# Performance work log

Hardware: AMD Instinct MI355X
Metric: run time of the kernel (lower is better)

Reference implementation:

```python
import jax, jax.numpy as jnp
import numpy as np

N = 20000; F = 2000; H1 = 256; H2 = 64; E = 320000
BN_EPS = 1e-5


def setup_inputs() -> dict:
    key = jax.random.key(0)
    ks = jax.random.split(key, 32)
    def w(k, shape, fan_in):
        return jax.random.normal(k, shape, jnp.float32) * (1.0 / np.sqrt(fan_in))
    inp = {
        'x': jax.random.normal(ks[0], (N, F), jnp.float32),
        's_src': jax.random.randint(ks[1], (E,), 0, N, jnp.int32),
        's_dst': jax.random.randint(ks[2], (E,), 0, N, jnp.int32),
        's_w': jax.random.uniform(ks[3], (E,), jnp.float32),
        'f_src': jax.random.randint(ks[4], (E,), 0, N, jnp.int32),
        'f_dst': jax.random.randint(ks[5], (E,), 0, N, jnp.int32),
        'f_w': jax.random.uniform(ks[6], (E,), jnp.float32),
        'Ws1': w(ks[7], (F, H1), F), 'bs1': jnp.zeros((H1,), jnp.float32),
        'Ws2': w(ks[8], (H1, H2), H1), 'bs2': jnp.zeros((H2,), jnp.float32),
        'Wf1': w(ks[9], (F, H1), F), 'bf1': jnp.zeros((H1,), jnp.float32),
        'Wf2': w(ks[10], (H1, H2), H1), 'bf2': jnp.zeros((H2,), jnp.float32),
        'Wc1': w(ks[11], (F, H1), F), 'bc1': jnp.zeros((H1,), jnp.float32),
        'Wc2': w(ks[12], (H1, H2), H1), 'bc2': jnp.zeros((H2,), jnp.float32),
        'Wa1': w(ks[13], (H2, 16), H2), 'ba1': jnp.zeros((16,), jnp.float32),
        'Wa2': w(ks[14], (16, 1), 16),
        'Wm': w(ks[15], (H2, H2), H2), 'bm': jnp.zeros((H2,), jnp.float32),
        'Wd': w(ks[16], (H2, H1), H2), 'bd': jnp.zeros((H1,), jnp.float32),
        'bn_g': jnp.ones((H1,), jnp.float32), 'bn_b': jnp.zeros((H1,), jnp.float32),
        'bn_rm': jnp.zeros((H1,), jnp.float32), 'bn_rv': jnp.ones((H1,), jnp.float32),
        'Wpi': w(ks[17], (H1, F), H1), 'bpi': jnp.zeros((F,), jnp.float32),
        'Wdp': w(ks[18], (H1, F), H1), 'bdp': jnp.zeros((F,), jnp.float32),
        'Wmu': w(ks[19], (H1, F), H1), 'bmu': jnp.zeros((F,), jnp.float32),
    }
    return inp


def _spmm(src, dst, ew, h):
    # out[i] = sum over edges (j->i) ew * h[j]   (sparse adj @ dense)
    return jax.ops.segment_sum(h[src] * ew[:, None], dst, num_segments=N)


def _gcn(x, src, dst, ew, W1, b1, W2, b2):
    h = jax.nn.relu(_spmm(src, dst, ew, x @ W1) + b1)
    # dropout p=0 in eval -> identity
    return _spmm(src, dst, ew, h @ W2) + b2


def reference(x, s_src, s_dst, s_w, f_src, f_dst, f_w,
              Ws1, bs1, Ws2, bs2, Wf1, bf1, Wf2, bf2, Wc1, bc1, Wc2, bc2,
              Wa1, ba1, Wa2, Wm, bm, Wd, bd, bn_g, bn_b, bn_rm, bn_rv,
              Wpi, bpi, Wdp, bdp, Wmu, bmu):
    emb1 = _gcn(x, s_src, s_dst, s_w, Ws1, bs1, Ws2, bs2)   # SGCN on sadj
    emb2 = _gcn(x, f_src, f_dst, f_w, Wf1, bf1, Wf2, bf2)   # FGCN on fadj
    # CGCN applied to both graphs (com_comb is computed but unused in original)
    _ = _gcn(x, s_src, s_dst, s_w, Wc1, bc1, Wc2, bc2)
    _ = _gcn(x, f_src, f_dst, f_w, Wc1, bc1, Wc2, bc2)
    z = jnp.stack([emb1, emb2], axis=1)                     # [N, 2, H2]
    att_logits = jnp.tanh(z @ Wa1 + ba1) @ Wa2              # [N, 2, 1]
    beta = jax.nn.softmax(att_logits, axis=1)
    emb = (beta * z).sum(axis=1)                            # [N, H2]
    emb = emb @ Wm + bm                                     # MLP
    # ZINB decoder: Linear -> BatchNorm1d (eval) -> ReLU
    h = emb @ Wd + bd
    h = (h - bn_rm) * jax.lax.rsqrt(bn_rv + BN_EPS) * bn_g + bn_b
    h = jax.nn.relu(h)
    pi = jax.nn.sigmoid(h @ Wpi + bpi)
    disp = jnp.clip(jax.nn.softplus(h @ Wdp + bdp), 1e-4, 1e4)
    mean = jax.nn.sigmoid(h @ Wmu + bmu)
    return (emb1, emb2, emb, pi, disp, mean)
```

## Files before the change

### kernel.cpp

```cpp
#include <hip/hip_runtime.h>


typedef unsigned short bfu;
typedef __bf16 bf16x8 __attribute__((ext_vector_type(8)));
typedef float  f32x4  __attribute__((ext_vector_type(4)));

__device__ __forceinline__ float b2f(bfu u) {
    return __uint_as_float(((unsigned)u) << 16);
}
__device__ __forceinline__ bfu f2b(float f) {
    unsigned u = __float_as_uint(f);
    return (bfu)((u + 0x7FFFu + ((u >> 16) & 1u)) >> 16);
}
__device__ __forceinline__ float ldm(const void* p, size_t i, int bf) {
    return bf ? b2f(((const bfu*)p)[i]) : ((const float*)p)[i];
}
__device__ __forceinline__ void stm(void* p, size_t i, float v, int bf) {
    if (bf) ((bfu*)p)[i] = f2b(v);
    else    ((float*)p)[i] = v;
}

__global__ void detect_dtype_k(const unsigned* __restrict__ sw, int* __restrict__ flag) {
    __shared__ int cnt;
    if (threadIdx.x == 0) cnt = 0;
    __syncthreads();
    unsigned w = sw[threadIdx.x];
    if ((w & 0xFFFFu) >= 0x3F80u) atomicAdd(&cnt, 1);
    __syncthreads();
    if (threadIdx.x == 0) *flag = (cnt < 25) ? 1 : 0;
}

enum { EPI_F32 = 0, EPI_SIG = 1, EPI_SP = 2 };

__global__ __launch_bounds__(256) void transpose_bf16_k(
    const bfu* __restrict__ in, bfu* __restrict__ out, int R, int C,
    const int* __restrict__ flag)
{
    if (!*flag) return;
    __shared__ bfu tile[64][66];
    int r0 = blockIdx.x * 64, c0 = blockIdx.y * 64;
    int tx = threadIdx.x & 63, ty = threadIdx.x >> 6;
    for (int i = ty; i < 64; i += 4) {
        int r = r0 + i, c = c0 + tx;
        tile[i][tx] = (r < R && c < C) ? in[(size_t)r * C + c] : (bfu)0;
    }
    __syncthreads();
    for (int i = ty; i < 64; i += 4) {
        int c = c0 + i, r = r0 + tx;
        if (c < C && r < R) out[(size_t)c * R + r] = tile[tx][i];
    }
}

template <int EPI>
__global__ __launch_bounds__(256) void gemm_mfma(
    const bfu* __restrict__ A, const bfu* __restrict__ Bt,
    const void* __restrict__ bias,
    float* __restrict__ Cf, void* __restrict__ Cb, size_t cb_off,
    int M, int K, int Nn, const int* __restrict__ flag)
{
    if (!*flag) return;
    __shared__ __align__(16) bfu As[128 * 72];
    __shared__ __align__(16) bfu Bs[128 * 72];

    const int t = threadIdx.x;
    const int bm0 = blockIdx.x * 128, bn0 = blockIdx.y * 128;
    const int lane = t & 63, wid = t >> 6;
    const int wm = (wid >> 1) * 64, wn = (wid & 1) * 64;
    const int lr = lane & 15;
    const int lk = (lane >> 4) * 8;
    const int lq = (lane >> 4) * 4;

    f32x4 acc[4][4] = {};

    const int srow = t >> 3;
    const int skoff = (t & 7) * 8;

    for (int k0 = 0; k0 < K; k0 += 64) {
        int4 va[4], vb[4];
        #pragma unroll
        for (int h = 0; h < 4; h++) {
            int row = srow + h * 32;
            int gk = k0 + skoff;
            va[h] = make_int4(0, 0, 0, 0);
            vb[h] = make_int4(0, 0, 0, 0);
            int gm = bm0 + row;
            if (gm < M && gk < K)
                va[h] = *(const int4*)(A + (size_t)gm * K + gk);
            int gn = bn0 + row;
            if (gn < Nn && gk < K)
                vb[h] = *(const int4*)(Bt + (size_t)gn * K + gk);
        }
        __syncthreads();
        #pragma unroll
        for (int h = 0; h < 4; h++) {
            int row = srow + h * 32;
            *(int4*)&As[row * 72 + skoff] = va[h];
            *(int4*)&Bs[row * 72 + skoff] = vb[h];
        }
        __syncthreads();

        #pragma unroll
        for (int kk = 0; kk < 2; kk++) {
            bf16x8 af[4], bq[4];
            #pragma unroll
            for (int i = 0; i < 4; i++) {
                af[i] = *(const bf16x8*)&As[(wm + i * 16 + lr) * 72 + kk * 32 + lk];
                bq[i] = *(const bf16x8*)&Bs[(wn + i * 16 + lr) * 72 + kk * 32 + lk];
            }
            #pragma unroll
            for (int i = 0; i < 4; i++)
                #pragma unroll
                for (int j = 0; j < 4; j++)
                    acc[i][j] = __builtin_amdgcn_mfma_f32_16x16x32_bf16(
                        af[i], bq[j], acc[i][j], 0, 0, 0);
        }
    }

    #pragma unroll
    for (int j = 0; j < 4; j++) {
        int col = bn0 + wn + j * 16 + lr;
        if (col >= Nn) continue;
        #pragma unroll
        for (int i = 0; i < 4; i++) {
            #pragma unroll
            for (int r = 0; r < 4; r++) {
                int row = bm0 + wm + i * 16 + lq + r;
                if (row >= M) continue;
                float v = acc[i][j][r];
                if constexpr (EPI == EPI_F32) {
                    Cf[(size_t)row * Nn + col] = v;
                } else if constexpr (EPI == EPI_SIG) {
                    v += ldm(bias, col, 1);
                    v = 1.f / (1.f + __expf(-v));
                    stm(Cb, cb_off + (size_t)row * Nn + col, v, 1);
                } else {
                    v += ldm(bias, col, 1);
                    float sp = (v > 20.f) ? v : log1pf(__expf(v));
                    sp = fminf(fmaxf(sp, 1e-4f), 1e4f);
                    stm(Cb, cb_off + (size_t)row * Nn + col, sp, 1);
                }
            }
        }
    }
}

template <bool AGLB, int EPI, bool FP32ONLY>
__global__ __launch_bounds__(256) void gemm_tiled(
    const void* __restrict__ A, const void* __restrict__ B,
    const void* __restrict__ bias,
    float* __restrict__ Cf, void* __restrict__ Cb, size_t cb_off,
    int M, int K, int Nn, const int* __restrict__ flag)
{
    __shared__ __align__(16) float As[16][68];
    __shared__ __align__(16) float Bs[16][68];

    const int bf = *flag;
    if (FP32ONLY && bf) return;
    const int t = threadIdx.x;
    const int bm0 = blockIdx.x * 64, bn0 = blockIdx.y * 64;
    const int tx = t & 15, ty = t >> 4;

    const int am = t >> 2;
    const int ak = (t & 3) * 4;
    const int gm = bm0 + am;
    const bool arow = gm < M;
    const int bk = t >> 4;
    const int bn = (t & 15) * 4;
    const bool bcol = (bn0 + bn + 3) < Nn;

    float acc[4][4] = {};

    for (int k0 = 0; k0 < K; k0 += 16) {
        float av0 = 0.f, av1 = 0.f, av2 = 0.f, av3 = 0.f;
        float bv0 = 0.f, bv1 = 0.f, bv2 = 0.f, bv3 = 0.f;
        if (arow) {
            size_t off = (size_t)gm * K + k0 + ak;
            if (AGLB && bf) {
                ushort4 v = *(const ushort4*)((const bfu*)A + off);
                av0 = b2f(v.x); av1 = b2f(v.y); av2 = b2f(v.z); av3 = b2f(v.w);
            } else {
                float4 v = *(const float4*)((const float*)A + off);
                av0 = v.x; av1 = v.y; av2 = v.z; av3 = v.w;
            }
        }
        if (bcol) {
            size_t off = (size_t)(k0 + bk) * Nn + bn0 + bn;
            if (bf) {
                ushort4 v = *(const ushort4*)((const bfu*)B + off);
                bv0 = b2f(v.x); bv1 = b2f(v.y); bv2 = b2f(v.z); bv3 = b2f(v.w);
            } else {
                float4 v = *(const float4*)((const float*)B + off);
                bv0 = v.x; bv1 = v.y; bv2 = v.z; bv3 = v.w;
            }
        }

        __syncthreads();
        As[ak + 0][am] = av0; As[ak + 1][am] = av1;
        As[ak + 2][am] = av2; As[ak + 3][am] = av3;
        *(float4*)&Bs[bk][bn] = make_float4(bv0, bv1, bv2, bv3);
        __syncthreads();

        #pragma unroll
        for (int k = 0; k < 16; k++) {
            float4 a4 = *(const float4*)&As[k][ty * 4];
            float4 b4 = *(const float4*)&Bs[k][tx * 4];
            float aa[4] = {a4.x, a4.y, a4.z, a4.w};
            float bb[4] = {b4.x, b4.y, b4.z, b4.w};
            #pragma unroll
            for (int i = 0; i < 4; i++)
                #pragma unroll
                for (int j = 0; j < 4; j++)
                    acc[i][j] += aa[i] * bb[j];
        }
    }

    #pragma unroll
    for (int i = 0; i < 4; i++) {
        int row = bm0 + ty * 4 + i;
        if (row >= M) continue;
        #pragma unroll
        for (int j = 0; j < 4; j++) {
            int col = bn0 + tx * 4 + j;
            if (col >= Nn) continue;
            float v = acc[i][j];
            if constexpr (EPI == EPI_F32) {
                Cf[(size_t)row * Nn + col] = v;
            } else if constexpr (EPI == EPI_SIG) {
                v += ldm(bias, col, bf);
                v = 1.f / (1.f + __expf(-v));
                stm(Cb, cb_off + (size_t)row * Nn + col, v, bf);
            } else {
                v += ldm(bias, col, bf);
                float sp = (v > 20.f) ? v : log1pf(__expf(v));
                sp = fminf(fmaxf(sp, 1e-4f), 1e4f);
                stm(Cb, cb_off + (size_t)row * Nn + col, sp, bf);
            }
        }
    }
}

__global__ __launch_bounds__(256) void spmm_scatter(
    const float* __restrict__ Hin, const int* __restrict__ src,
    const int* __restrict__ dst, const void* __restrict__ w,
    float* __restrict__ outp, int E, int C, const int* __restrict__ flag)
{
    int bf = *flag;
    int gw = (blockIdx.x * 256 + threadIdx.x) >> 6;
    int lane = threadIdx.x & 63;
    if (gw >= E) return;
    int s = src[gw], d = dst[gw];
    float ww = ldm(w, gw, bf);
    const float* hp = Hin + (size_t)s * C;
    float* op = outp + (size_t)d * C;
    for (int c = lane; c < C; c += 64)
        atomicAdd(&op[c], ww * hp[c]);
}

__global__ __launch_bounds__(256) void bias_relu_k(
    float* __restrict__ H, const void* __restrict__ bias, int total, int Cm1,
    const int* __restrict__ flag)
{
    int bf = *flag;
    int i = blockIdx.x * 256 + threadIdx.x;
    if (i >= total) return;
    float v = H[i] + ldm(bias, i & Cm1, bf);
    H[i] = fmaxf(v, 0.f);
}

__global__ __launch_bounds__(256) void bias_store_emb_k(
    float* __restrict__ Ef, const void* __restrict__ bias,
    void* __restrict__ outb, size_t out_off, int total,
    const int* __restrict__ flag)
{
    int bf = *flag;
    int i = blockIdx.x * 256 + threadIdx.x;
    if (i >= total) return;
    float v = Ef[i] + ldm(bias, i & 63, bf);
    Ef[i] = v;
    stm(outb, out_off + i, v, bf);
}

__global__ __launch_bounds__(256) void bn_relu_k(
    float* __restrict__ H, const void* __restrict__ bd,
    const void* __restrict__ g, const void* __restrict__ b,
    const void* __restrict__ rm, const void* __restrict__ rv,
    bfu* __restrict__ hb, int total, const int* __restrict__ flag)
{
    int bf = *flag;
    int i = blockIdx.x * 256 + threadIdx.x;
    if (i >= total) return;
    int c = i & 255;
    float v = H[i] + ldm(bd, c, bf);
    v = (v - ldm(rm, c, bf)) * rsqrtf(ldm(rv, c, bf) + 1e-5f) * ldm(g, c, bf)
        + ldm(b, c, bf);
    v = fmaxf(v, 0.f);
    H[i] = v;
    if (bf) hb[i] = f2b(v);
}

__global__ __launch_bounds__(256) void attn_mlp_k(
    const float* __restrict__ E1, const float* __restrict__ E2,
    const void* __restrict__ Wa1, const void* __restrict__ ba1,
    const void* __restrict__ Wa2,
    const void* __restrict__ Wm, const void* __restrict__ bm,
    float* __restrict__ Eout, void* __restrict__ outb, size_t out_off,
    const int* __restrict__ flag)
{
    __shared__ float sh[4][3][64];
    int bf = *flag;
    int wid = threadIdx.x >> 6, lane = threadIdx.x & 63;
    int node = blockIdx.x * 4 + wid;

    float e1 = E1[(size_t)node * 64 + lane];
    float e2 = E2[(size_t)node * 64 + lane];
    sh[wid][0][lane] = e1;
    sh[wid][1][lane] = e2;
    __syncthreads();

    float part = 0.f;
    if (lane < 32) {
        int tt = lane & 15;
        const float* es = sh[wid][lane >> 4];
        float a = 0.f;
        for (int m = 0; m < 64; m++) a += es[m] * ldm(Wa1, m * 16 + tt, bf);
        part = tanhf(a + ldm(ba1, tt, bf)) * ldm(Wa2, tt, bf);
    }
    part += __shfl_xor(part, 1);
    part += __shfl_xor(part, 2);
    part += __shfl_xor(part, 4);
    part += __shfl_xor(part, 8);
    float lg1 = __shfl(part, 0);
    float lg2 = __shfl(part, 16);
    float mx = fmaxf(lg1, lg2);
    float p1 = __expf(lg1 - mx), p2 = __expf(lg2 - mx);
    float inv = 1.f / (p1 + p2);
    float comb = (p1 * inv) * e1 + (p2 * inv) * e2;
    sh[wid][2][lane] = comb;
    __syncthreads();

    const float* cs = sh[wid][2];
    float acc = ldm(bm, lane, bf);
    for (int m = 0; m < 64; m++) acc += cs[m] * ldm(Wm, m * 64 + lane, bf);
    size_t idx = (size_t)node * 64 + lane;
    Eout[idx] = acc;
    stm(outb, out_off + idx, acc, bf);
}

extern "C" void kernel_launch(void* const* d_in, const int* in_sizes, int n_in,
                              void* d_out, int out_size, void* d_ws, size_t ws_size,
                              hipStream_t stream)
{
    const int N = 20000, F = 2000, H1 = 256, H2 = 64, E = 320000, FOUT = 2000;

    const void* x     = d_in[0];
    const int* s_src = (const int*)d_in[1];
    const int* s_dst = (const int*)d_in[2];
    const void* s_w   = d_in[3];
    const int* f_src = (const int*)d_in[4];
    const int* f_dst = (const int*)d_in[5];
    const void* f_w   = d_in[6];
    const void *Ws1 = d_in[7],  *bs1 = d_in[8];
    const void *Ws2 = d_in[9],  *bs2 = d_in[10];
    const void *Wf1 = d_in[11], *bf1 = d_in[12];
    const void *Wf2 = d_in[13], *bf2 = d_in[14];
    const void *Wa1 = d_in[19], *ba1 = d_in[20];
    const void *Wa2 = d_in[21];
    const void *Wm  = d_in[22], *bm  = d_in[23];
    const void *Wd  = d_in[24], *bd  = d_in[25];
    const void *bn_g = d_in[26], *bn_b = d_in[27];
    const void *bn_rm = d_in[28], *bn_rv = d_in[29];
    const void *Wpi = d_in[30], *bpi = d_in[31];
    const void *Wdp = d_in[32], *bdp = d_in[33];
    const void *Wmu = d_in[34], *bmu = d_in[35];

    const size_t o_emb1 = 0;
    const size_t o_emb2 = (size_t)N * H2;
    const size_t o_emb  = 2 * (size_t)N * H2;
    const size_t o_pi   = 3 * (size_t)N * H2;
    const size_t o_disp = o_pi + (size_t)N * FOUT;
    const size_t o_mean = o_disp + (size_t)N * FOUT;

    char* wsb = (char*)d_ws;
    int* flag = (int*)wsb;
    float* XW  = (float*)(wsb + 256);
    float* H   = XW + (size_t)N * H1;
    float* G2  = H  + (size_t)N * H1;
    float* e1f = G2 + (size_t)N * H2;
    float* e2f = e1f + (size_t)N * H2;
    float* emf = e2f + (size_t)N * H2;
    float* hdec = XW;
    bfu* hdec_bf = (bfu*)H;
    bfu* Bt      = (bfu*)G2;

    const int MB  = (N + 63) / 64;
    const int MB2 = (N + 127) / 128;

    detect_dtype_k<<<1, 256, 0, stream>>>((const unsigned*)s_w, flag);

    transpose_bf16_k<<<dim3(32, 4), 256, 0, stream>>>(
        (const bfu*)Ws1, Bt, F, H1, flag);
    gemm_mfma<EPI_F32><<<dim3(MB2, 2), 256, 0, stream>>>(
        (const bfu*)x, Bt, nullptr, XW, nullptr, 0, N, F, H1, flag);
    gemm_tiled<true, EPI_F32, true><<<dim3(MB, 4), 256, 0, stream>>>(
        x, Ws1, nullptr, XW, nullptr, 0, N, F, H1, flag);
    hipMemsetAsync(H, 0, (size_t)N * H1 * 4, stream);
    spmm_scatter<<<E / 4, 256, 0, stream>>>(XW, s_src, s_dst, s_w, H, E, H1, flag);
    bias_relu_k<<<(N * H1) / 256, 256, 0, stream>>>(H, bs1, N * H1, H1 - 1, flag);
    gemm_tiled<false, EPI_F32, false><<<dim3(MB, 1), 256, 0, stream>>>(
        H, Ws2, nullptr, G2, nullptr, 0, N, H1, H2, flag);
    hipMemsetAsync(e1f, 0, (size_t)N * H2 * 4, stream);
    spmm_scatter<<<E / 4, 256, 0, stream>>>(G2, s_src, s_dst, s_w, e1f, E, H2, flag);
    bias_store_emb_k<<<(N * H2) / 256, 256, 0, stream>>>(
        e1f, bs2, d_out, o_emb1, N * H2, flag);

    transpose_bf16_k<<<dim3(32, 4), 256, 0, stream>>>(
        (const bfu*)Wf1, Bt, F, H1, flag);
    gemm_mfma<EPI_F32><<<dim3(MB2, 2), 256, 0, stream>>>(
        (const bfu*)x, Bt, nullptr, XW, nullptr, 0, N, F, H1, flag);
    gemm_tiled<true, EPI_F32, true><<<dim3(MB, 4), 256, 0, stream>>>(
        x, Wf1, nullptr, XW, nullptr, 0, N, F, H1, flag);
    hipMemsetAsync(H, 0, (size_t)N * H1 * 4, stream);
    spmm_scatter<<<E / 4, 256, 0, stream>>>(XW, f_src, f_dst, f_w, H, E, H1, flag);
    bias_relu_k<<<(N * H1) / 256, 256, 0, stream>>>(H, bf1, N * H1, H1 - 1, flag);
    gemm_tiled<false, EPI_F32, false><<<dim3(MB, 1), 256, 0, stream>>>(
        H, Wf2, nullptr, G2, nullptr, 0, N, H1, H2, flag);
    hipMemsetAsync(e2f, 0, (size_t)N * H2 * 4, stream);
    spmm_scatter<<<E / 4, 256, 0, stream>>>(G2, f_src, f_dst, f_w, e2f, E, H2, flag);
    bias_store_emb_k<<<(N * H2) / 256, 256, 0, stream>>>(
        e2f, bf2, d_out, o_emb2, N * H2, flag);

    attn_mlp_k<<<N / 4, 256, 0, stream>>>(
        e1f, e2f, Wa1, ba1, Wa2, Wm, bm, emf, d_out, o_emb, flag);

    gemm_tiled<false, EPI_F32, false><<<dim3(MB, 4), 256, 0, stream>>>(
        emf, Wd, nullptr, hdec, nullptr, 0, N, H2, H1, flag);
    bn_relu_k<<<(N * H1) / 256, 256, 0, stream>>>(
        hdec, bd, bn_g, bn_b, bn_rm, bn_rv, hdec_bf, N * H1, flag);

    transpose_bf16_k<<<dim3(4, 32), 256, 0, stream>>>(
        (const bfu*)Wpi, Bt, H1, FOUT, flag);
    gemm_mfma<EPI_SIG><<<dim3(MB2, 16), 256, 0, stream>>>(
        hdec_bf, Bt, bpi, nullptr, d_out, o_pi, N, H1, FOUT, flag);
    gemm_tiled<false, EPI_SIG, true><<<dim3(MB, 32), 256, 0, stream>>>(
        hdec, Wpi, bpi, nullptr, d_out, o_pi, N, H1, FOUT, flag);
    transpose_bf16_k<<<dim3(4, 32), 256, 0, stream>>>(
        (const bfu*)Wdp, Bt, H1, FOUT, flag);
    gemm_mfma<EPI_SP><<<dim3(MB2, 16), 256, 0, stream>>>(
        hdec_bf, Bt, bdp, nullptr, d_out, o_disp, N, H1, FOUT, flag);
    gemm_tiled<false, EPI_SP, true><<<dim3(MB, 32), 256, 0, stream>>>(
        hdec, Wdp, bdp, nullptr, d_out, o_disp, N, H1, FOUT, flag);
    transpose_bf16_k<<<dim3(4, 32), 256, 0, stream>>>(
        (const bfu*)Wmu, Bt, H1, FOUT, flag);
    gemm_mfma<EPI_SIG><<<dim3(MB2, 16), 256, 0, stream>>>(
        hdec_bf, Bt, bmu, nullptr, d_out, o_mean, N, H1, FOUT, flag);
    gemm_tiled<false, EPI_SIG, true><<<dim3(MB, 32), 256, 0, stream>>>(
        hdec, Wmu, bmu, nullptr, d_out, o_mean, N, H1, FOUT, flag);
}
```

Measured before the change: 2.852 ms.

## Replace fp32 SIMT GEMMs with split-bf16 three-term MFMA GEMMs

For the fp32 input path, the large GEMMs (x@W1 and the three ZINB output heads) move from a scalar tiled fp32 kernel to MFMA bf16 kernels. Each fp32 operand is split into hi and lo bf16 parts, and three MFMA products (hh, hl, lh) are summed to approximate fp32 accuracy. Weights are transposed and split by a new kernel, and the decoder activation is split inside bn_relu. The MFMA path costs three times the matrix ops and extra LDS (four buffers) in exchange for avoiding slow fp32 FMA throughput, and it carries some accuracy risk relative to true fp32.

```diff
diff --git a/kernel.cpp b/kernel.cpp
--- a/kernel.cpp
+++ b/kernel.cpp
@@ -18,6 +18,12 @@
 __device__ __forceinline__ void stm(void* p, size_t i, float v, int bf) {
     if (bf) ((bfu*)p)[i] = f2b(v);
     else    ((float*)p)[i] = v;
+}
+__device__ __forceinline__ void splitf(float f, bfu& h, bfu& l) {
+    unsigned u = __float_as_uint(f);
+    h = (bfu)(u >> 16);
+    float r = f - __uint_as_float(u & 0xFFFF0000u);
+    l = f2b(r);
 }
 
 __global__ void detect_dtype_k(const unsigned* __restrict__ sw, int* __restrict__ flag) {
@@ -48,6 +54,30 @@
     for (int i = ty; i < 64; i += 4) {
         int c = c0 + i, r = r0 + tx;
         if (c < C && r < R) out[(size_t)c * R + r] = tile[tx][i];
+    }
+}
+
+__global__ __launch_bounds__(256) void transpose_split_f32_k(
+    const float* __restrict__ in, bfu* __restrict__ ohi, bfu* __restrict__ olo,
+    int R, int C, const int* __restrict__ flag)
+{
+    if (*flag) return;
+    __shared__ float tile[64][65];
+    int r0 = blockIdx.x * 64, c0 = blockIdx.y * 64;
+    int tx = threadIdx.x & 63, ty = threadIdx.x >> 6;
+    for (int i = ty; i < 64; i += 4) {
+        int r = r0 + i, c = c0 + tx;
+        tile[i][tx] = (r < R && c < C) ? in[(size_t)r * C + c] : 0.f;
+    }
+    __syncthreads();
+    for (int i = ty; i < 64; i += 4) {
+        int c = c0 + i, r = r0 + tx;
+        if (c < C && r < R) {
+            float v = tile[tx][i];
+            bfu h, l; splitf(v, h, l);
+            ohi[(size_t)c * R + r] = h;
+            olo[(size_t)c * R + r] = l;
+        }
     }
 }
 
@@ -144,9 +174,156 @@
     }
 }
 
-template <bool AGLB, int EPI, bool FP32ONLY>
+template <int EPI, bool APRE>
+__global__ __launch_bounds__(256, 2) void gemm_mfma_split(
+    const float* __restrict__ Af,
+    const bfu* __restrict__ Ah, const bfu* __restrict__ Al,
+    const bfu* __restrict__ Bth, const bfu* __restrict__ Btl,
+    const float* __restrict__ bias,
+    float* __restrict__ Cf, float* __restrict__ Cb, size_t cb_off,
+    int M, int K, int Nn, const int* __restrict__ flag)
+{
+    if (*flag) return;
+    __shared__ __align__(16) bfu Ash[128 * 72];
+    __shared__ __align__(16) bfu Asl[128 * 72];
+    __shared__ __align__(16) bfu Bsh[128 * 72];
+    __shared__ __align__(16) bfu Bsl[128 * 72];
+
+    const int t = threadIdx.x;
+    const int bm0 = blockIdx.x * 128, bn0 = blockIdx.y * 128;
+    const int lane = t & 63, wid = t >> 6;
+    const int wm = (wid >> 1) * 64, wn = (wid & 1) * 64;
+    const int lr = lane & 15;
+    const int lk = (lane >> 4) * 8;
+    const int lq = (lane >> 4) * 4;
+
+    f32x4 acc[4][4] = {};
+
+    const int srow = t >> 1;
+    const int scol = (t & 1) * 32;
+    const int gm = bm0 + srow;
+    const int gn = bn0 + srow;
+    const bool amok = gm < M;
+    const bool bnok = gn < Nn;
+
+    for (int k0 = 0; k0 < K; k0 += 64) {
+        float4 va[8];
+        int4 vah[4], val[4];
+        int4 vbh[4], vbl[4];
+        if constexpr (!APRE) {
+            #pragma unroll
+            for (int c = 0; c < 8; c++) {
+                int gk = k0 + scol + c * 4;
+                va[c] = make_float4(0.f, 0.f, 0.f, 0.f);
+                if (amok && gk < K)
+                    va[c] = *(const float4*)(Af + (size_t)gm * K + gk);
+            }
+        } else {
+            #pragma unroll
+            for (int c = 0; c < 4; c++) {
+                int gk = k0 + scol + c * 8;
+                vah[c] = make_int4(0, 0, 0, 0);
+                val[c] = make_int4(0, 0, 0, 0);
+                if (amok && gk < K) {
+                    vah[c] = *(const int4*)(Ah + (size_t)gm * K + gk);
+                    val[c] = *(const int4*)(Al + (size_t)gm * K + gk);
+                }
+            }
+        }
+        #pragma unroll
+        for (int c = 0; c < 4; c++) {
+            int gk = k0 + scol + c * 8;
+            vbh[c] = make_int4(0, 0, 0, 0);
+            vbl[c] = make_int4(0, 0, 0, 0);
+            if (bnok && gk < K) {
+                vbh[c] = *(const int4*)(Bth + (size_t)gn * K + gk);
+                vbl[c] = *(const int4*)(Btl + (size_t)gn * K + gk);
+            }
+        }
+
+        __syncthreads();
+        if constexpr (!APRE) {
+            #pragma unroll
+            for (int c = 0; c < 8; c++) {
+                ushort4 hv, lv;
+                splitf(va[c].x, hv.x, lv.x);
+                splitf(va[c].y, hv.y, lv.y);
+                splitf(va[c].z, hv.z, lv.z);
+                splitf(va[c].w, hv.w, lv.w);
+                *(ushort4*)&Ash[srow * 72 + scol + c * 4] = hv;
+                *(ushort4*)&Asl[srow * 72 + scol + c * 4] = lv;
+            }
+        } else {
+            #pragma unroll
+            for (int c = 0; c < 4; c++) {
+                *(int4*)&Ash[srow * 72 + scol + c * 8] = vah[c];
+                *(int4*)&Asl[srow * 72 + scol + c * 8] = val[c];
+            }
+        }
+        #pragma unroll
+        for (int c = 0; c < 4; c++) {
+            *(int4*)&Bsh[srow * 72 + scol + c * 8] = vbh[c];
+            *(int4*)&Bsl[srow * 72 + scol + c * 8] = vbl[c];
+        }
+        __syncthreads();
+
+        #pragma unroll
+        for (int kk = 0; kk < 2; kk++) {
+            bf16x8 ah[4], al4[4], bh[4], bl4[4];
+            #pragma unroll
+            for (int i = 0; i < 4; i++) {
+                int ao = (wm + i * 16 + lr) * 72 + kk * 32 + lk;
+                int bo = (wn + i * 16 + lr) * 72 + kk * 32 + lk;
+                ah[i]  = *(const bf16x8*)&Ash[ao];
+                al4[i] = *(const bf16x8*)&Asl[ao];
+                bh[i]  = *(const bf16x8*)&Bsh[bo];
+                bl4[i] = *(const bf16x8*)&Bsl[bo];
+            }
+            #pragma unroll
+            for (int i = 0; i < 4; i++)
+                #pragma unroll
+                for (int j = 0; j < 4; j++) {
+                    acc[i][j] = __builtin_amdgcn_mfma_f32_16x16x32_bf16(
+                        ah[i], bh[j], acc[i][j], 0, 0, 0);
+                    acc[i][j] = __builtin_amdgcn_mfma_f32_16x16x32_bf16(
+                        ah[i], bl4[j], acc[i][j], 0, 0, 0);
+                    acc[i][j] = __builtin_amdgcn_mfma_f32_16x16x32_bf16(
+                        al4[i], bh[j], acc[i][j], 0, 0, 0);
+                }
+        }
+    }
+
+    #pragma unroll
+    for (int j = 0; j < 4; j++) {
+        int col = bn0 + wn + j * 16 + lr;
+        if (col >= Nn) continue;
+        #pragma unroll
+        for (int i = 0; i < 4; i++) {
+            #pragma unroll
+            for (int r = 0; r < 4; r++) {
+                int row = bm0 + wm + i * 16 + lq + r;
+                if (row >= M) continue;
+                float v = acc[i][j][r];
+                if constexpr (EPI == EPI_F32) {
+                    Cf[(size_t)row * Nn + col] = v;
+                } else if constexpr (EPI == EPI_SIG) {
+                    v += bias[col];
+                    v = 1.f / (1.f + __expf(-v));
+                    Cb[cb_off + (size_t)row * Nn + col] = v;
+                } else {
+                    v += bias[col];
+                    float sp = (v > 20.f) ? v : log1pf(__expf(v));
+                    sp = fminf(fmaxf(sp, 1e-4f), 1e4f);
+                    Cb[cb_off + (size_t)row * Nn + col] = sp;
+                }
+            }
+        }
+    }
+}
+
+template <int EPI>
 __global__ __launch_bounds__(256) void gemm_tiled(
-    const void* __restrict__ A, const void* __restrict__ B,
+    const float* __restrict__ A, const void* __restrict__ B,
     const void* __restrict__ bias,
     float* __restrict__ Cf, void* __restrict__ Cb, size_t cb_off,
     int M, int K, int Nn, const int* __restrict__ flag)
@@ -155,7 +332,6 @@
     __shared__ __align__(16) float Bs[16][68];
 
     const int bf = *flag;
-    if (FP32ONLY && bf) return;
     const int t = threadIdx.x;
     const int bm0 = blockIdx.x * 64, bn0 = blockIdx.y * 64;
     const int tx = t & 15, ty = t >> 4;
@@ -175,13 +351,8 @@
         float bv0 = 0.f, bv1 = 0.f, bv2 = 0.f, bv3 = 0.f;
         if (arow) {
             size_t off = (size_t)gm * K + k0 + ak;
-            if (AGLB && bf) {
-                ushort4 v = *(const ushort4*)((const bfu*)A + off);
-                av0 = b2f(v.x); av1 = b2f(v.y); av2 = b2f(v.z); av3 = b2f(v.w);
-            } else {
-                float4 v = *(const float4*)((const float*)A + off);
-                av0 = v.x; av1 = v.y; av2 = v.z; av3 = v.w;
-            }
+            float4 v = *(const float4*)(A + off);
+            av0 = v.x; av1 = v.y; av2 = v.z; av3 = v.w;
         }
         if (bcol) {
             size_t off = (size_t)(k0 + bk) * Nn + bn0 + bn;
@@ -284,7 +455,8 @@
     float* __restrict__ H, const void* __restrict__ bd,
     const void* __restrict__ g, const void* __restrict__ b,
     const void* __restrict__ rm, const void* __restrict__ rv,
-    bfu* __restrict__ hb, int total, const int* __restrict__ flag)
+    bfu* __restrict__ hb, bfu* __restrict__ lb, int total,
+    const int* __restrict__ flag)
 {
     int bf = *flag;
     int i = blockIdx.x * 256 + threadIdx.x;
@@ -295,7 +467,9 @@
         + ldm(b, c, bf);
     v = fmaxf(v, 0.f);
     H[i] = v;
-    if (bf) hb[i] = f2b(v);
+    bfu h = f2b(v);
+    hb[i] = h;
+    if (!bf) lb[i] = f2b(v - b2f(h));
 }
 
 __global__ __launch_bounds__(256) void attn_mlp_k(
@@ -389,8 +563,10 @@
     float* e2f = e1f + (size_t)N * H2;
     float* emf = e2f + (size_t)N * H2;
     float* hdec = XW;
-    bfu* hdec_bf = (bfu*)H;
-    bfu* Bt      = (bfu*)G2;
+    bfu* Bt_hi = (bfu*)G2;
+    bfu* Bt_lo = Bt_hi + (size_t)F * H1;
+    bfu* hdec_hi = (bfu*)H;
+    bfu* hdec_lo = hdec_hi + (size_t)N * H1;
 
     const int MB  = (N + 63) / 64;
     const int MB2 = (N + 127) / 128;
@@ -398,15 +574,18 @@
     detect_dtype_k<<<1, 256, 0, stream>>>((const unsigned*)s_w, flag);
 
     transpose_bf16_k<<<dim3(32, 4), 256, 0, stream>>>(
-        (const bfu*)Ws1, Bt, F, H1, flag);
+        (const bfu*)Ws1, Bt_hi, F, H1, flag);
+    transpose_split_f32_k<<<dim3(32, 4), 256, 0, stream>>>(
+        (const float*)Ws1, Bt_hi, Bt_lo, F, H1, flag);
     gemm_mfma<EPI_F32><<<dim3(MB2, 2), 256, 0, stream>>>(
-        (const bfu*)x, Bt, nullptr, XW, nullptr, 0, N, F, H1, flag);
-    gemm_tiled<true, EPI_F32, true><<<dim3(MB, 4), 256, 0, stream>>>(
-        x, Ws1, nullptr, XW, nullptr, 0, N, F, H1, flag);
+        (const bfu*)x, Bt_hi, nullptr, XW, nullptr, 0, N, F, H1, flag);
+    gemm_mfma_split<EPI_F32, false><<<dim3(MB2, 2), 256, 0, stream>>>(
+        (const float*)x, nullptr, nullptr, Bt_hi, Bt_lo, nullptr,
+        XW, nullptr, 0, N, F, H1, flag);
     hipMemsetAsync(H, 0, (size_t)N * H1 * 4, stream);
     spmm_scatter<<<E / 4, 256, 0, stream>>>(XW, s_src, s_dst, s_w, H, E, H1, flag);
     bias_relu_k<<<(N * H1) / 256, 256, 0, stream>>>(H, bs1, N * H1, H1 - 1, flag);
-    gemm_tiled<false, EPI_F32, false><<<dim3(MB, 1), 256, 0, stream>>>(
+    gemm_tiled<EPI_F32><<<dim3(MB, 1), 256, 0, stream>>>(
         H, Ws2, nullptr, G2, nullptr, 0, N, H1, H2, flag);
     hipMemsetAsync(e1f, 0, (size_t)N * H2 * 4, stream);
     spmm_scatter<<<E / 4, 256, 0, stream>>>(G2, s_src, s_dst, s_w, e1f, E, H2, flag);
@@ -414,15 +593,18 @@
         e1f, bs2, d_out, o_emb1, N * H2, flag);
 
     transpose_bf16_k<<<dim3(32, 4), 256, 0, stream>>>(
-        (const bfu*)Wf1, Bt, F, H1, flag);
+        (const bfu*)Wf1, Bt_hi, F, H1, flag);
+    transpose_split_f32_k<<<dim3(32, 4), 256, 0, stream>>>(
+        (const float*)Wf1, Bt_hi, Bt_lo, F, H1, flag);
     gemm_mfma<EPI_F32><<<dim3(MB2, 2), 256, 0, stream>>>(
-        (const bfu*)x, Bt, nullptr, XW, nullptr, 0, N, F, H1, flag);
-    gemm_tiled<true, EPI_F32, true><<<dim3(MB, 4), 256, 0, stream>>>(
-        x, Wf1, nullptr, XW, nullptr, 0, N, F, H1, flag);
+        (const bfu*)x, Bt_hi, nullptr, XW, nullptr, 0, N, F, H1, flag);
+    gemm_mfma_split<EPI_F32, false><<<dim3(MB2, 2), 256, 0, stream>>>(
+        (const float*)x, nullptr, nullptr, Bt_hi, Bt_lo, nullptr,
+        XW, nullptr, 0, N, F, H1, flag);
     hipMemsetAsync(H, 0, (size_t)N * H1 * 4, stream);
     spmm_scatter<<<E / 4, 256, 0, stream>>>(XW, f_src, f_dst, f_w, H, E, H1, flag);
     bias_relu_k<<<(N * H1) / 256, 256, 0, stream>>>(H, bf1, N * H1, H1 - 1, flag);
-    gemm_tiled<false, EPI_F32, false><<<dim3(MB, 1), 256, 0, stream>>>(
+    gemm_tiled<EPI_F32><<<dim3(MB, 1), 256, 0, stream>>>(
         H, Wf2, nullptr, G2, nullptr, 0, N, H1, H2, flag);
     hipMemsetAsync(e2f, 0, (size_t)N * H2 * 4, stream);
     spmm_scatter<<<E / 4, 256, 0, stream>>>(G2, f_src, f_dst, f_w, e2f, E, H2, flag);
@@ -432,27 +614,36 @@
     attn_mlp_k<<<N / 4, 256, 0, stream>>>(
         e1f, e2f, Wa1, ba1, Wa2, Wm, bm, emf, d_out, o_emb, flag);
 
-    gemm_tiled<false, EPI_F32, false><<<dim3(MB, 4), 256, 0, stream>>>(
+    gemm_tiled<EPI_F32><<<dim3(MB, 4), 256, 0, stream>>>(
         emf, Wd, nullptr, hdec, nullptr, 0, N, H2, H1, flag);
     bn_relu_k<<<(N * H1) / 256, 256, 0, stream>>>(
-        hdec, bd, bn_g, bn_b, bn_rm, bn_rv, hdec_bf, N * H1, flag);
+        hdec, bd, bn_g, bn_b, bn_rm, bn_rv, hdec_hi, hdec_lo, N * H1, flag);
 
     transpose_bf16_k<<<dim3(4, 32), 256, 0, stream>>>(
-        (const bfu*)Wpi, Bt, H1, FOUT, flag);
+        (const bfu*)Wpi, Bt_hi, H1, FOUT, flag);
+    transpose_split_f32_k<<<dim3(4, 32), 256, 0, stream>>>(
+        (const float*)Wpi, Bt_hi, Bt_lo, H1, FOUT, flag);
     gemm_mfma<EPI_SIG><<<dim3(MB2, 16), 256, 0, stream>>>(
-        hdec_bf, Bt, bpi, nullptr, d_out, o_pi, N, H1, FOUT, flag);
-    gemm_tiled<false, EPI_SIG, true><<<dim3(MB, 32), 256, 0, stream>>>(
-        hdec, Wpi, bpi, nullptr, d_out, o_pi, N, H1, FOUT, flag);
+        hdec_hi, Bt_hi, bpi, nullptr, d_out, o_pi, N, H1, FOUT, flag);
+    gemm_mfma_split<EPI_SIG, true><<<dim3(MB2, 16), 256, 0, stream>>>(
+        nullptr, hdec_hi, hdec_lo, Bt_hi, Bt_lo, (const float*)bpi,
+        nullptr, (float*)d_out, o_pi, N, H1, FOUT, flag);
     transpose_bf16_k<<<dim3(4, 32), 256, 0, stream>>>(
-        (const bfu*)Wdp, Bt, H1, FOUT, flag);
+        (const bfu*)Wdp, Bt_hi, H1, FOUT, flag);
+    transpose_split_f32_k<<<dim3(4, 32), 256, 0, stream>>>(
+        (const float*)Wdp, Bt_hi, Bt_lo, H1, FOUT, flag);
     gemm_mfma<EPI_SP><<<dim3(MB2, 16), 256, 0, stream>>>(
-        hdec_bf, Bt, bdp, nullptr, d_out, o_disp, N, H1, FOUT, flag);
-    gemm_tiled<false, EPI_SP, true><<<dim3(MB, 32), 256, 0, stream>>>(
-        hdec, Wdp, bdp, nullptr, d_out, o_disp, N, H1, FOUT, flag);
+        hdec_hi, Bt_hi, bdp, nullptr, d_out, o_disp, N, H1, FOUT, flag);
+    gemm_mfma_split<EPI_SP, true><<<dim3(MB2, 16), 256, 0, stream>>>(
+        nullptr, hdec_hi, hdec_lo, Bt_hi, Bt_lo, (const float*)bdp,
+        nullptr, (float*)d_out, o_disp, N, H1, FOUT, flag);
     transpose_bf16_k<<<dim3(4, 32), 256, 0, stream>>>(
-        (const bfu*)Wmu, Bt, H1, FOUT, flag);
+        (const bfu*)Wmu, Bt_hi, H1, FOUT, flag);
+    transpose_split_f32_k<<<dim3(4, 32), 256, 0, stream>>>(
+        (const float*)Wmu, Bt_hi, Bt_lo, H1, FOUT, flag);
     gemm_mfma<EPI_SIG><<<dim3(MB2, 16), 256, 0, stream>>>(
-        hdec_bf, Bt, bmu, nullptr, d_out, o_mean, N, H1, FOUT, flag);
-    gemm_tiled<false, EPI_SIG, true><<<dim3(MB, 32), 256, 0, stream>>>(
-        hdec, Wmu, bmu, nullptr, d_out, o_mean, N, H1, FOUT, flag);
-}
+        hdec_hi, Bt_hi, bmu, nullptr, d_out, o_mean, N, H1, FOUT, flag);
+    gemm_mfma_split<EPI_SIG, true><<<dim3(MB2, 16), 256, 0, stream>>>(
+        nullptr, hdec_hi, hdec_lo, Bt_hi, Bt_lo, (const float*)bmu,
+        nullptr, (float*)d_out, o_mean, N, H1, FOUT, flag);
+}
```

Measured after the change: 2.495 ms. -12.5%, faster.
